# Optimization experiments

Hardware: AMD Instinct MI355X
Metric: run time of the kernel (lower is better)

## Reference

```python
import jax, jax.numpy as jnp
import numpy as np

DIM = 128
B, N = 2, 72


def setup_inputs() -> dict:
    key = jax.random.key(0)
    ks = jax.random.split(key, 6)
    s = 1.0 / np.sqrt(DIM)
    s3 = 1.0 / np.sqrt(3 * DIM)
    return {
        "node_emb": jax.random.normal(ks[0], (B * N, DIM), dtype=jnp.float32),
        "path_emb": jax.random.normal(ks[1], (B, N, N, DIM), dtype=jnp.float32),
        "W_hz": jax.random.uniform(ks[2], (DIM, DIM), minval=-s, maxval=s, dtype=jnp.float32),
        "b_hz": jax.random.uniform(ks[3], (DIM,), minval=-s, maxval=s, dtype=jnp.float32),
        "W_zz": jax.random.uniform(ks[4], (3 * DIM, DIM), minval=-s3, maxval=s3, dtype=jnp.float32),
        "b_zz": jax.random.uniform(ks[5], (DIM,), minval=-s3, maxval=s3, dtype=jnp.float32),
    }


def reference(node_emb, path_emb, W_hz, b_hz, W_zz, b_zz):
    b, n, _, d = path_emb.shape
    # z = W_hz(path_emb)
    z = jnp.einsum('bijd,de->bije', path_emb, W_hz) + b_hz
    # tropical (max-plus) triangle aggregation: out[b,i,j,d] = max_k z[b,i,k,d] + z[b,k,j,d]
    z_conv = jnp.max(z[:, :, :, None, :] + z[:, None, :, :, :], axis=2)  # (b,n,n,d)
    # path_aggr with mode 'max' -> elementwise max of z_conv and z
    z = jnp.maximum(z_conv, z)
    ne = node_emb.reshape(b, n, d)
    n_i = jnp.broadcast_to(ne[:, :, None, :], (b, n, n, d))
    n_j = jnp.broadcast_to(ne[:, None, :, :], (b, n, n, d))
    zc = jnp.concatenate([n_i, z, n_j], axis=-1)  # (b,n,n,3d)
    out = jax.nn.relu(jnp.einsum('bijc,ce->bije', zc, W_zz) + b_zz)
    return out
```

## Files before the change

kernel.cpp:

```cpp
#include <hip/hip_runtime.h>

#define DIM 128
#define NN 72
#define BB 2
#define NROWS (BB*NN*NN)
#define BN (BB*NN)
#define ZBLOCKS (NROWS/16)

__global__ __launch_bounds__(256) void k_phase1(const float* __restrict__ path,
                                                const float* __restrict__ Whz,
                                                const float* __restrict__ bhz,
                                                float* __restrict__ z,
                                                const float* __restrict__ node,
                                                const float* __restrict__ Wzz,
                                                float* __restrict__ P1,
                                                float* __restrict__ P3) {
    __shared__ float rows[16 * DIM];
    const int t = threadIdx.x;

    if (blockIdx.x < ZBLOCKS) {
        const int r0 = blockIdx.x * 16;
        {
            float4* rs = (float4*)rows;
            const float4* pg = (const float4*)(path + r0 * DIM);
            rs[t]       = pg[t];
            rs[t + 256] = pg[t + 256];
        }
        __syncthreads();

        const int e2 = t & 63;
        const int rg = t >> 6;
        float2 bz = *(const float2*)&bhz[2 * e2];
        float2 acc[4];
#pragma unroll
        for (int r = 0; r < 4; r++) acc[r] = bz;

        const float* Wp = Whz + 2 * e2;
        float2 w[4], wn[4];
#pragma unroll
        for (int dd = 0; dd < 4; dd++) w[dd] = *(const float2*)&Wp[dd * DIM];

        for (int d4 = 0; d4 < DIM / 4; d4++) {
            if (d4 < DIM / 4 - 1) {
#pragma unroll
                for (int dd = 0; dd < 4; dd++)
                    wn[dd] = *(const float2*)&Wp[(4 * d4 + 4 + dd) * DIM];
            }
            float4 pr[4];
#pragma unroll
            for (int r = 0; r < 4; r++)
                pr[r] = *(const float4*)&rows[(rg + 4 * r) * DIM + 4 * d4];
#pragma unroll
            for (int dd = 0; dd < 4; dd++)
#pragma unroll
                for (int r = 0; r < 4; r++) {
                    float pv = ((const float*)&pr[r])[dd];
                    acc[r].x = fmaf(pv, w[dd].x, acc[r].x);
                    acc[r].y = fmaf(pv, w[dd].y, acc[r].y);
                }
#pragma unroll
            for (int dd = 0; dd < 4; dd++) w[dd] = wn[dd];
        }
#pragma unroll
        for (int r = 0; r < 4; r++)
            *(float2*)&z[(r0 + rg + 4 * r) * DIM + 2 * e2] = acc[r];
    } else {
        const int r0 = (blockIdx.x - ZBLOCKS) * 8;
        {
            float4* rs = (float4*)rows;
            const float4* ng = (const float4*)(node + r0 * DIM);
            rs[t] = ng[t];
        }
        __syncthreads();
        const int e  = t & 127;
        const int rr = t >> 7;
        float a1[4] = {0.f, 0.f, 0.f, 0.f};
        float a3[4] = {0.f, 0.f, 0.f, 0.f};
        const float* W1 = Wzz + e;
        const float* W3 = Wzz + 2 * DIM * DIM + e;
        for (int d = 0; d < DIM; d++) {
            float w1 = W1[d * DIM];
            float w3 = W3[d * DIM];
#pragma unroll
            for (int s = 0; s < 4; s++) {
                float pv = rows[(rr + 2 * s) * DIM + d];
                a1[s] = fmaf(pv, w1, a1[s]);
                a3[s] = fmaf(pv, w3, a3[s]);
            }
        }
#pragma unroll
        for (int s = 0; s < 4; s++) {
            int m = r0 + rr + 2 * s;
            P1[m * DIM + e] = a1[s];
            P3[m * DIM + e] = a3[s];
        }
    }
}

__global__ __launch_bounds__(256, 4) void k_trop_out(
        const float* __restrict__ z,   const float* __restrict__ Wzz,
        const float* __restrict__ bzz, const float* __restrict__ P1,
        const float* __restrict__ P3,  float* __restrict__ out) {
    __shared__ float rows[16 * DIM];
    __shared__ float comb[16 * DIM];
    const int t   = threadIdx.x;
    const int blk = blockIdx.x;
    const int b   = blk / 324;
    const int rem = blk - b * 324;
    const int it  = rem / 18;
    const int jt  = rem - it * 18;
    const int i0 = it * 4, j0 = jt * 4;
    const int d  = t & 127;
    const int ty = t >> 7;
    const float* zb = z + b * NN * NN * DIM;

    {
        float acc[16];
#pragma unroll
        for (int q = 0; q < 16; q++) acc[q] = -3.402823466e38f;

        float zi[4], zj[4], zin[4], zjn[4];
        int k = ty;
#pragma unroll
        for (int a = 0; a < 4; a++) zi[a] = zb[((i0 + a) * NN + k) * DIM + d];
#pragma unroll
        for (int c = 0; c < 4; c++) zj[c] = zb[(k * NN + (j0 + c)) * DIM + d];

        for (int it2 = 0; it2 < NN / 2; it2++) {
            int kn = k + 2;
            if (it2 < NN / 2 - 1) {
#pragma unroll
                for (int a = 0; a < 4; a++) zin[a] = zb[((i0 + a) * NN + kn) * DIM + d];
#pragma unroll
                for (int c = 0; c < 4; c++) zjn[c] = zb[(kn * NN + (j0 + c)) * DIM + d];
            }
#pragma unroll
            for (int a = 0; a < 4; a++)
#pragma unroll
                for (int c = 0; c < 4; c++)
                    acc[a * 4 + c] = fmaxf(acc[a * 4 + c], zi[a] + zj[c]);
#pragma unroll
            for (int a = 0; a < 4; a++) { zi[a] = zin[a]; zj[a] = zjn[a]; }
            k = kn;
        }

        if (ty == 1) {
#pragma unroll
            for (int q = 0; q < 16; q++) comb[q * DIM + d] = acc[q];
        }
        __syncthreads();
        if (ty == 0) {
#pragma unroll
            for (int a = 0; a < 4; a++)
#pragma unroll
                for (int c = 0; c < 4; c++) {
                    int q = a * 4 + c;
                    float m = fmaxf(acc[q], comb[q * DIM + d]);
                    int idx = ((i0 + a) * NN + (j0 + c)) * DIM + d;
                    rows[q * DIM + d] = fmaxf(m, zb[idx]);
                }
        }
    }
    __syncthreads();

    {
        const int e2 = t & 63;
        const int rg = t >> 6;
        float2 acc[4];
#pragma unroll
        for (int r = 0; r < 4; r++) acc[r] = make_float2(0.f, 0.f);

        const float* Wp = Wzz + DIM * DIM + 2 * e2;
        float2 w[4], wn[4];
#pragma unroll
        for (int dd = 0; dd < 4; dd++) w[dd] = *(const float2*)&Wp[dd * DIM];
        for (int d4 = 0; d4 < DIM / 4; d4++) {
            if (d4 < DIM / 4 - 1) {
#pragma unroll
                for (int dd = 0; dd < 4; dd++)
                    wn[dd] = *(const float2*)&Wp[(4 * d4 + 4 + dd) * DIM];
            }
            float4 pr[4];
#pragma unroll
            for (int r = 0; r < 4; r++)
                pr[r] = *(const float4*)&rows[(rg + 4 * r) * DIM + 4 * d4];
#pragma unroll
            for (int dd = 0; dd < 4; dd++)
#pragma unroll
                for (int r = 0; r < 4; r++) {
                    float pv = ((const float*)&pr[r])[dd];
                    acc[r].x = fmaf(pv, w[dd].x, acc[r].x);
                    acc[r].y = fmaf(pv, w[dd].y, acc[r].y);
                }
#pragma unroll
            for (int dd = 0; dd < 4; dd++) w[dd] = wn[dd];
        }

        float2 bz = *(const float2*)&bzz[2 * e2];
#pragma unroll
        for (int r = 0; r < 4; r++) {
            int q = rg + 4 * r;
            int a = q >> 2, c = q & 3;
            int orow = b * NN * NN + (i0 + a) * NN + (j0 + c);
            float2 v1 = *(const float2*)&P1[(b * NN + i0 + a) * DIM + 2 * e2];
            float2 v3 = *(const float2*)&P3[(b * NN + j0 + c) * DIM + 2 * e2];
            float ox = fmaxf(acc[r].x + v1.x + v3.x + bz.x, 0.f);
            float oy = fmaxf(acc[r].y + v1.y + v3.y + bz.y, 0.f);
            *(float2*)&out[orow * DIM + 2 * e2] = make_float2(ox, oy);
        }
    }
}

extern "C" void kernel_launch(void* const* d_in, const int* in_sizes, int n_in,
                              void* d_out, int out_size, void* d_ws, size_t ws_size,
                              hipStream_t stream) {
    const float* node = (const float*)d_in[0];
    const float* path = (const float*)d_in[1];
    const float* Whz  = (const float*)d_in[2];
    const float* bhz  = (const float*)d_in[3];
    const float* Wzz  = (const float*)d_in[4];
    const float* bzz  = (const float*)d_in[5];
    float* out = (float*)d_out;

    float* z  = (float*)d_ws;
    float* P1 = z + NROWS * DIM;
    float* P3 = P1 + BN * DIM;

    hipLaunchKernelGGL(k_phase1,   dim3(ZBLOCKS + 18), dim3(256), 0, stream,
                       path, Whz, bhz, z, node, Wzz, P1, P3);
    hipLaunchKernelGGL(k_trop_out, dim3(BB * 18 * 18), dim3(256), 0, stream,
                       z, Wzz, bzz, P1, P3, out);
}
```

Before: 109.6 us.

## Write transposed z copy and batch k-loop loads in tropical aggregation

Phase 1 now also writes a transposed copy zT, so the max-plus kernel can read z[k,j] as zT[j,k]. Both operands then stride the same way along k. The tropical loop now prefetches four k-steps per iteration (32 values in flight), and both GEMM inner loops are unrolled to eight-wide d steps. Occupancy bounds change to 4 and 3 blocks. The cost is an extra full-size z write plus much higher register use in the trop kernel.

New measurement: 107.2 us. 2.3% less time.

```diff
diff --git a/kernel.cpp b/kernel.cpp
--- a/kernel.cpp
+++ b/kernel.cpp
@@ -3,18 +3,20 @@
 #define DIM 128
 #define NN 72
 #define BB 2
-#define NROWS (BB*NN*NN)
+#define NSQ (NN*NN)
+#define NROWS (BB*NSQ)
 #define BN (BB*NN)
 #define ZBLOCKS (NROWS/16)
 
-__global__ __launch_bounds__(256) void k_phase1(const float* __restrict__ path,
-                                                const float* __restrict__ Whz,
-                                                const float* __restrict__ bhz,
-                                                float* __restrict__ z,
-                                                const float* __restrict__ node,
-                                                const float* __restrict__ Wzz,
-                                                float* __restrict__ P1,
-                                                float* __restrict__ P3) {
+__global__ __launch_bounds__(256, 4) void k_phase1(const float* __restrict__ path,
+                                                   const float* __restrict__ Whz,
+                                                   const float* __restrict__ bhz,
+                                                   float* __restrict__ z,
+                                                   float* __restrict__ zT,
+                                                   const float* __restrict__ node,
+                                                   const float* __restrict__ Wzz,
+                                                   float* __restrict__ P1,
+                                                   float* __restrict__ P3) {
     __shared__ float rows[16 * DIM];
     const int t = threadIdx.x;
 
@@ -36,34 +38,55 @@
         for (int r = 0; r < 4; r++) acc[r] = bz;
 
         const float* Wp = Whz + 2 * e2;
-        float2 w[4], wn[4];
-#pragma unroll
-        for (int dd = 0; dd < 4; dd++) w[dd] = *(const float2*)&Wp[dd * DIM];
-
-        for (int d4 = 0; d4 < DIM / 4; d4++) {
-            if (d4 < DIM / 4 - 1) {
-#pragma unroll
-                for (int dd = 0; dd < 4; dd++)
-                    wn[dd] = *(const float2*)&Wp[(4 * d4 + 4 + dd) * DIM];
-            }
-            float4 pr[4];
-#pragma unroll
-            for (int r = 0; r < 4; r++)
-                pr[r] = *(const float4*)&rows[(rg + 4 * r) * DIM + 4 * d4];
-#pragma unroll
-            for (int dd = 0; dd < 4; dd++)
-#pragma unroll
-                for (int r = 0; r < 4; r++) {
-                    float pv = ((const float*)&pr[r])[dd];
-                    acc[r].x = fmaf(pv, w[dd].x, acc[r].x);
-                    acc[r].y = fmaf(pv, w[dd].y, acc[r].y);
-                }
-#pragma unroll
-            for (int dd = 0; dd < 4; dd++) w[dd] = wn[dd];
-        }
-#pragma unroll
-        for (int r = 0; r < 4; r++)
-            *(float2*)&z[(r0 + rg + 4 * r) * DIM + 2 * e2] = acc[r];
+        float2 w0[4], w1[4], n0[4], n1[4];
+#pragma unroll
+        for (int dd = 0; dd < 4; dd++) {
+            w0[dd] = *(const float2*)&Wp[dd * DIM];
+            w1[dd] = *(const float2*)&Wp[(4 + dd) * DIM];
+        }
+        for (int d8 = 0; d8 < 16; d8++) {
+            if (d8 < 15) {
+#pragma unroll
+                for (int dd = 0; dd < 4; dd++) {
+                    n0[dd] = *(const float2*)&Wp[(8 * d8 + 8 + dd) * DIM];
+                    n1[dd] = *(const float2*)&Wp[(8 * d8 + 12 + dd) * DIM];
+                }
+            }
+            float4 pa[4], pb[4];
+#pragma unroll
+            for (int r = 0; r < 4; r++) {
+                pa[r] = *(const float4*)&rows[(rg + 4 * r) * DIM + 8 * d8];
+                pb[r] = *(const float4*)&rows[(rg + 4 * r) * DIM + 8 * d8 + 4];
+            }
+#pragma unroll
+            for (int dd = 0; dd < 4; dd++)
+#pragma unroll
+                for (int r = 0; r < 4; r++) {
+                    float pv = ((const float*)&pa[r])[dd];
+                    acc[r].x = fmaf(pv, w0[dd].x, acc[r].x);
+                    acc[r].y = fmaf(pv, w0[dd].y, acc[r].y);
+                }
+#pragma unroll
+            for (int dd = 0; dd < 4; dd++)
+#pragma unroll
+                for (int r = 0; r < 4; r++) {
+                    float pv = ((const float*)&pb[r])[dd];
+                    acc[r].x = fmaf(pv, w1[dd].x, acc[r].x);
+                    acc[r].y = fmaf(pv, w1[dd].y, acc[r].y);
+                }
+#pragma unroll
+            for (int dd = 0; dd < 4; dd++) { w0[dd] = n0[dd]; w1[dd] = n1[dd]; }
+        }
+#pragma unroll
+        for (int r = 0; r < 4; r++) {
+            int row = r0 + rg + 4 * r;
+            *(float2*)&z[row * DIM + 2 * e2] = acc[r];
+            int b  = row / NSQ;
+            int ij = row - b * NSQ;
+            int i  = ij / NN;
+            int j  = ij - i * NN;
+            *(float2*)&zT[(b * NSQ + j * NN + i) * DIM + 2 * e2] = acc[r];
+        }
     } else {
         const int r0 = (blockIdx.x - ZBLOCKS) * 8;
         {
@@ -97,10 +120,11 @@
     }
 }
 
-__global__ __launch_bounds__(256, 4) void k_trop_out(
-        const float* __restrict__ z,   const float* __restrict__ Wzz,
-        const float* __restrict__ bzz, const float* __restrict__ P1,
-        const float* __restrict__ P3,  float* __restrict__ out) {
+__global__ __launch_bounds__(256, 3) void k_trop_out(
+        const float* __restrict__ z,   const float* __restrict__ zT,
+        const float* __restrict__ Wzz, const float* __restrict__ bzz,
+        const float* __restrict__ P1,  const float* __restrict__ P3,
+        float* __restrict__ out) {
     __shared__ float rows[16 * DIM];
     __shared__ float comb[16 * DIM];
     const int t   = threadIdx.x;
@@ -112,36 +136,46 @@
     const int i0 = it * 4, j0 = jt * 4;
     const int d  = t & 127;
     const int ty = t >> 7;
-    const float* zb = z + b * NN * NN * DIM;
+    const float* zb  = z  + b * NSQ * DIM;
+    const float* zTb = zT + b * NSQ * DIM;
 
     {
         float acc[16];
 #pragma unroll
         for (int q = 0; q < 16; q++) acc[q] = -3.402823466e38f;
 
-        float zi[4], zj[4], zin[4], zjn[4];
-        int k = ty;
-#pragma unroll
-        for (int a = 0; a < 4; a++) zi[a] = zb[((i0 + a) * NN + k) * DIM + d];
-#pragma unroll
-        for (int c = 0; c < 4; c++) zj[c] = zb[(k * NN + (j0 + c)) * DIM + d];
-
-        for (int it2 = 0; it2 < NN / 2; it2++) {
-            int kn = k + 2;
-            if (it2 < NN / 2 - 1) {
-#pragma unroll
-                for (int a = 0; a < 4; a++) zin[a] = zb[((i0 + a) * NN + kn) * DIM + d];
-#pragma unroll
-                for (int c = 0; c < 4; c++) zjn[c] = zb[(kn * NN + (j0 + c)) * DIM + d];
-            }
-#pragma unroll
-            for (int a = 0; a < 4; a++)
-#pragma unroll
-                for (int c = 0; c < 4; c++)
-                    acc[a * 4 + c] = fmaxf(acc[a * 4 + c], zi[a] + zj[c]);
-#pragma unroll
-            for (int a = 0; a < 4; a++) { zi[a] = zin[a]; zj[a] = zjn[a]; }
-            k = kn;
+        float cur[32], nxt[32];
+#pragma unroll
+        for (int kk = 0; kk < 4; kk++) {
+            int k = ty + 2 * kk;
+#pragma unroll
+            for (int s = 0; s < 4; s++) {
+                cur[kk * 8 + s]     = zb [((i0 + s) * NN + k) * DIM + d];
+                cur[kk * 8 + 4 + s] = zTb[((j0 + s) * NN + k) * DIM + d];
+            }
+        }
+        for (int g = 0; g < 9; g++) {
+            if (g < 8) {
+#pragma unroll
+                for (int kk = 0; kk < 4; kk++) {
+                    int k = ty + 2 * kk + 8 * (g + 1);
+#pragma unroll
+                    for (int s = 0; s < 4; s++) {
+                        nxt[kk * 8 + s]     = zb [((i0 + s) * NN + k) * DIM + d];
+                        nxt[kk * 8 + 4 + s] = zTb[((j0 + s) * NN + k) * DIM + d];
+                    }
+                }
+            }
+#pragma unroll
+            for (int kk = 0; kk < 4; kk++)
+#pragma unroll
+                for (int a = 0; a < 4; a++)
+#pragma unroll
+                    for (int c = 0; c < 4; c++)
+                        acc[a * 4 + c] = fmaxf(acc[a * 4 + c],
+                                               cur[kk * 8 + a] + cur[kk * 8 + 4 + c]);
+#pragma unroll
+            for (int q = 0; q < 32; q++) cur[q] = nxt[q];
         }
 
         if (ty == 1) {
@@ -171,29 +205,44 @@
         for (int r = 0; r < 4; r++) acc[r] = make_float2(0.f, 0.f);
 
         const float* Wp = Wzz + DIM * DIM + 2 * e2;
-        float2 w[4], wn[4];
-#pragma unroll
-        for (int dd = 0; dd < 4; dd++) w[dd] = *(const float2*)&Wp[dd * DIM];
-        for (int d4 = 0; d4 < DIM / 4; d4++) {
-            if (d4 < DIM / 4 - 1) {
-#pragma unroll
-                for (int dd = 0; dd < 4; dd++)
-                    wn[dd] = *(const float2*)&Wp[(4 * d4 + 4 + dd) * DIM];
-            }
-            float4 pr[4];
-#pragma unroll
-            for (int r = 0; r < 4; r++)
-                pr[r] = *(const float4*)&rows[(rg + 4 * r) * DIM + 4 * d4];
-#pragma unroll
-            for (int dd = 0; dd < 4; dd++)
-#pragma unroll
-                for (int r = 0; r < 4; r++) {
-                    float pv = ((const float*)&pr[r])[dd];
-                    acc[r].x = fmaf(pv, w[dd].x, acc[r].x);
-                    acc[r].y = fmaf(pv, w[dd].y, acc[r].y);
-                }
-#pragma unroll
-            for (int dd = 0; dd < 4; dd++) w[dd] = wn[dd];
+        float2 w0[4], w1[4], n0[4], n1[4];
+#pragma unroll
+        for (int dd = 0; dd < 4; dd++) {
+            w0[dd] = *(const float2*)&Wp[dd * DIM];
+            w1[dd] = *(const float2*)&Wp[(4 + dd) * DIM];
+        }
+        for (int d8 = 0; d8 < 16; d8++) {
+            if (d8 < 15) {
+#pragma unroll
+                for (int dd = 0; dd < 4; dd++) {
+                    n0[dd] = *(const float2*)&Wp[(8 * d8 + 8 + dd) * DIM];
+                    n1[dd] = *(const float2*)&Wp[(8 * d8 + 12 + dd) * DIM];
+                }
+            }
+            float4 pa[4], pb[4];
+#pragma unroll
+            for (int r = 0; r < 4; r++) {
+                pa[r] = *(const float4*)&rows[(rg + 4 * r) * DIM + 8 * d8];
+                pb[r] = *(const float4*)&rows[(rg + 4 * r) * DIM + 8 * d8 + 4];
+            }
+#pragma unroll
+            for (int dd = 0; dd < 4; dd++)
+#pragma unroll
+                for (int r = 0; r < 4; r++) {
+                    float pv = ((const float*)&pa[r])[dd];
+                    acc[r].x = fmaf(pv, w0[dd].x, acc[r].x);
+                    acc[r].y = fmaf(pv, w0[dd].y, acc[r].y);
+                }
+#pragma unroll
+            for (int dd = 0; dd < 4; dd++)
+#pragma unroll
+                for (int r = 0; r < 4; r++) {
+                    float pv = ((const float*)&pb[r])[dd];
+                    acc[r].x = fmaf(pv, w1[dd].x, acc[r].x);
+                    acc[r].y = fmaf(pv, w1[dd].y, acc[r].y);
+                }
+#pragma unroll
+            for (int dd = 0; dd < 4; dd++) { w0[dd] = n0[dd]; w1[dd] = n1[dd]; }
         }
 
         float2 bz = *(const float2*)&bzz[2 * e2];
@@ -201,7 +250,7 @@
         for (int r = 0; r < 4; r++) {
             int q = rg + 4 * r;
             int a = q >> 2, c = q & 3;
-            int orow = b * NN * NN + (i0 + a) * NN + (j0 + c);
+            int orow = b * NSQ + (i0 + a) * NN + (j0 + c);
             float2 v1 = *(const float2*)&P1[(b * NN + i0 + a) * DIM + 2 * e2];
             float2 v3 = *(const float2*)&P3[(b * NN + j0 + c) * DIM + 2 * e2];
             float ox = fmaxf(acc[r].x + v1.x + v3.x + bz.x, 0.f);
@@ -223,11 +272,12 @@
     float* out = (float*)d_out;
 
     float* z  = (float*)d_ws;
-    float* P1 = z + NROWS * DIM;
+    float* zT = z  + NROWS * DIM;
+    float* P1 = zT + NROWS * DIM;
     float* P3 = P1 + BN * DIM;
 
     hipLaunchKernelGGL(k_phase1,   dim3(ZBLOCKS + 18), dim3(256), 0, stream,
-                       path, Whz, bhz, z, node, Wzz, P1, P3);
+                       path, Whz, bhz, z, zT, node, Wzz, P1, P3);
     hipLaunchKernelGGL(k_trop_out, dim3(BB * 18 * 18), dim3(256), 0, stream,
-                       z, Wzz, bzz, P1, P3, out);
+                       z, zT, Wzz, bzz, P1, P3, out);
 }
```
